# Performance work log

Measured on AMD Instinct MI355X. Metric: run time of the kernel, lower is better.

## Reference

```python
import jax, jax.numpy as jnp
import numpy as np

H = 16          # num_heads
R = 4           # query compression ratio
WIN = 128       # sliding window size
NEG = -1e9      # finite mask value (safe softmax grads)


def setup_inputs() -> dict:
    key = jax.random.key(0)
    k0, k1, k2, k3, k4 = jax.random.split(key, 5)
    B, S, D = 4, 4096, 2048
    inputs = jax.random.normal(k0, (B, S, D), jnp.float32)
    attention_mask = jnp.ones((B, S), jnp.int32)
    s = 0.02
    Wq = jax.random.normal(k1, (D, D), jnp.float32) * s
    Wk = jax.random.normal(k2, (D, D), jnp.float32) * s
    Wv = jax.random.normal(k3, (D, D), jnp.float32) * s
    Wo = jax.random.normal(k4, (D, D), jnp.float32) * s
    return {"inputs": inputs, "attention_mask": attention_mask,
            "Wq": Wq, "Wk": Wk, "Wv": Wv, "Wo": Wo}


def _forward(inputs, attention_mask, Wq, Wk, Wv, Wo):
    B, S, D = inputs.shape
    dh = D // H
    scale = 1.0 / np.sqrt(dh).astype(np.float32)
    Cs = (S + R - 1) // R            # compressed query length (S % R == 0 here)
    win = min(WIN, S)
    ws = max(0, S - win)             # window start

    # Q projection -> [B,H,S,dh] -> compress groups of R by mean -> [B,H,Cs,dh]
    q = jnp.einsum('bsd,od->bso', inputs, Wq)
    q = q.reshape(B, S, H, dh).transpose(0, 2, 1, 3)
    qc = q.reshape(B, H, Cs, R, dh).mean(axis=3)

    # K/V only over the recent window
    wx = inputs[:, ws:ws + win, :]
    k = jnp.einsum('bsd,od->bso', wx, Wk).reshape(B, win, H, dh).transpose(0, 2, 1, 3)
    v = jnp.einsum('bsd,od->bso', wx, Wv).reshape(B, win, H, dh).transpose(0, 2, 1, 3)

    scores = jnp.einsum('bhqd,bhkd->bhqk', qc, k) * scale

    # causal mask: each compressed query sits at position (i+1)*R-1
    qpos = (jnp.arange(Cs) + 1) * R - 1                     # [Cs]
    wpos = ws + jnp.arange(win)
    causal = wpos[None, :] <= qpos[:, None]
    qbw = qpos < ws                                         # queries fully before window
    causal = causal.at[:, 0].set(causal[:, 0] | qbw)
    pad_ok = (attention_mask[:, ws:ws + win] != 0)
    full = causal[None, None, :, :] & pad_ok[:, None, None, :]

    scores = jnp.where(full, scores, NEG)
    weights = jax.nn.softmax(scores, axis=-1)
    out = jnp.einsum('bhqk,bhkd->bhqd', weights, v)         # [B,H,Cs,dh]
    out = out.transpose(0, 2, 1, 3).reshape(B, Cs, D)
    out = jnp.einsum('bsd,od->bso', out, Wo)

    if Cs != S:  # linear interpolation back to seq_len (align_corners=False)
        out = jax.image.resize(out, (B, S, D), method='linear')
    return out


def reference(inputs, attention_mask, Wq, Wk, Wv, Wo):
    return _forward(inputs, attention_mask, Wq, Wk, Wv, Wo)
```

## Files before the change

### kernel.cpp

```cpp
#include <hip/hip_runtime.h>
#include <hip/hip_bf16.h>


typedef __attribute__((ext_vector_type(8))) short short8;
typedef __attribute__((ext_vector_type(4))) float f32x4;

#define QP_SLICE  (128 * 2048)
#define KV_SLICE  (512 * 2048)
#define YO_STRIDE (132 * 2048)

__device__ __forceinline__ unsigned short f2bf(float f){
  unsigned int x = __float_as_uint(f);
  return (unsigned short)((x + 0x7fffu + ((x >> 16) & 1u)) >> 16);
}
__device__ __forceinline__ float bf2f(unsigned short u){
  return __uint_as_float(((unsigned int)u) << 16);
}
__device__ __forceinline__ float bflo(unsigned int u){ return __uint_as_float(u << 16); }
__device__ __forceinline__ float bfhi(unsigned int u){ return __uint_as_float(u & 0xffff0000u); }
__device__ __forceinline__ unsigned int pk2(float lo, float hi){
  return ((unsigned int)f2bf(hi) << 16) | (unsigned int)f2bf(lo);
}
__device__ __forceinline__ short8 cvt8(float4 x, float4 y){
  union { unsigned int u[4]; short8 s; } r;
  r.u[0] = pk2(x.x, x.y); r.u[1] = pk2(x.z, x.w);
  r.u[2] = pk2(y.x, y.y); r.u[3] = pk2(y.z, y.w);
  return r.s;
}

__global__ __launch_bounds__(256) void prep_kernel(
    const float* __restrict__ inp,
    const float* __restrict__ Wq, const float* __restrict__ Wk,
    const float* __restrict__ Wv, const float* __restrict__ Wo,
    unsigned short* __restrict__ Wb,
    unsigned short* __restrict__ Awx, unsigned short* __restrict__ Aq)
{
  const int bx = blockIdx.x;
  if (bx < 8192){
    const int idx = bx * 256 + threadIdx.x;
    const int w = idx >> 19;
    const int sub = idx & 524287;
    const float* src = (w == 0) ? Wq : (w == 1) ? Wk : (w == 2) ? Wv : Wo;
    const float* p = src + (size_t)sub * 8;
    *(short8*)&Wb[(size_t)w * 4194304 + (size_t)sub * 8] =
        cvt8(*(const float4*)p, *(const float4*)(p + 4));
  } else if (bx < 8704){
    const int idx = (bx - 8192) * 256 + threadIdx.x;
    const int b = idx >> 15;
    const int j = (idx >> 8) & 127;
    const int d8 = (idx & 255) * 8;
    const float* p = inp + ((size_t)b * 4096 + 3968 + j) * 2048 + d8;
    *(short8*)&Awx[((size_t)b * 128 + j) * 2048 + d8] =
        cvt8(*(const float4*)p, *(const float4*)(p + 4));
  } else {
    const int idx = (bx - 8704) * 256 + threadIdx.x;
    const int b = idx >> 13;
    const int c = (idx >> 8) & 31;
    const int d8 = (idx & 255) * 8;
    const float* p = inp + ((size_t)b * 4096 + 3968 + 4 * c) * 2048 + d8;
    float4 x0 = *(const float4*)(p);
    float4 x1 = *(const float4*)(p + 2048);
    float4 x2 = *(const float4*)(p + 4096);
    float4 x3 = *(const float4*)(p + 6144);
    float4 y0 = *(const float4*)(p + 4);
    float4 y1 = *(const float4*)(p + 2052);
    float4 y2 = *(const float4*)(p + 4100);
    float4 y3 = *(const float4*)(p + 6148);
    float4 xm, ym;
    xm.x = 0.25f * (x0.x + x1.x + x2.x + x3.x);
    xm.y = 0.25f * (x0.y + x1.y + x2.y + x3.y);
    xm.z = 0.25f * (x0.z + x1.z + x2.z + x3.z);
    xm.w = 0.25f * (x0.w + x1.w + x2.w + x3.w);
    ym.x = 0.25f * (y0.x + y1.x + y2.x + y3.x);
    ym.y = 0.25f * (y0.y + y1.y + y2.y + y3.y);
    ym.z = 0.25f * (y0.z + y1.z + y2.z + y3.z);
    ym.w = 0.25f * (y0.w + y1.w + y2.w + y3.w);
    *(short8*)&Aq[((size_t)b * 32 + c) * 2048 + d8] = cvt8(xm, ym);
  }
}

__device__ __forceinline__ void stage_tile(
    const unsigned short* __restrict__ A, const unsigned short* __restrict__ W,
    int row0, int n0, int kt,
    unsigned short* As, unsigned short* Bs, int wid, int lane)
{
  const int r  = lane >> 3;
  const int ug = ((lane & 7) ^ r) * 8;
  #pragma unroll
  for (int i = 0; i < 4; ++i){
    const int c = wid * 4 + i;
    __builtin_amdgcn_global_load_lds(
        (const __attribute__((address_space(1))) void*)(A + (size_t)(row0 + c * 8 + r) * 2048 + kt + ug),
        (__attribute__((address_space(3))) void*)(As + c * 512),
        16, 0, 0);
    __builtin_amdgcn_global_load_lds(
        (const __attribute__((address_space(1))) void*)(W + (size_t)(n0 + c * 8 + r) * 2048 + kt + ug),
        (__attribute__((address_space(3))) void*)(Bs + c * 512),
        16, 0, 0);
  }
}

template<bool OUT_BF16>
__device__ __forceinline__ void gemm_body(
    const unsigned short* __restrict__ A, const unsigned short* __restrict__ W,
    unsigned short* __restrict__ Cb, float* __restrict__ Cf,
    int M, int row0, int n0, int kbase, int nsteps,
    unsigned short* L)
{
  const int tid  = threadIdx.x;
  const int lane = tid & 63;
  const int wid  = tid >> 6;
  const int wr = wid >> 1, wc = wid & 1;

  f32x4 acc[4][4] = {};

  stage_tile(A, W, row0, n0, kbase, L, L + 8192, wid, lane);
  int cur = 0;

  for (int t = 0; t < nsteps; ++t){
    __syncthreads();
    const int nxt = cur ^ 1;
    if (t + 1 < nsteps)
      stage_tile(A, W, row0, n0, kbase + (t + 1) * 64,
                 L + nxt * 16384, L + nxt * 16384 + 8192, wid, lane);
    const unsigned short* As = L + cur * 16384;
    const unsigned short* Bs = As + 8192;
    #pragma unroll
    for (int ks = 0; ks < 2; ++ks){
      short8 av[4], bv[4];
      const int unit = ks * 4 + (lane >> 4);
      #pragma unroll
      for (int f = 0; f < 4; ++f){
        const int row = wr * 64 + f * 16 + (lane & 15);
        av[f] = *(const short8*)&As[row * 64 + ((unit ^ (row & 7)) * 8)];
      }
      #pragma unroll
      for (int n = 0; n < 4; ++n){
        const int row = wc * 64 + n * 16 + (lane & 15);
        bv[n] = *(const short8*)&Bs[row * 64 + ((unit ^ (row & 7)) * 8)];
      }
      #pragma unroll
      for (int f = 0; f < 4; ++f)
        #pragma unroll
        for (int n = 0; n < 4; ++n)
          acc[f][n] = __builtin_amdgcn_mfma_f32_16x16x32_bf16(av[f], bv[n], acc[f][n], 0, 0, 0);
    }
    cur = nxt;
  }

  #pragma unroll
  for (int f = 0; f < 4; ++f){
    #pragma unroll
    for (int n = 0; n < 4; ++n){
      const int col = n0 + wc * 64 + n * 16 + (lane & 15);
      #pragma unroll
      for (int r = 0; r < 4; ++r){
        const int row = row0 + wr * 64 + f * 16 + (lane >> 4) * 4 + r;
        if (row < M){
          if (OUT_BF16) Cb[(size_t)row * 2048 + col] = f2bf(acc[f][n][r]);
          else          Cf[(size_t)row * 2048 + col] = acc[f][n][r];
        }
      }
    }
  }
}

__global__ __launch_bounds__(256, 2) void qkv_kernel(
    const unsigned short* __restrict__ Aq, const unsigned short* __restrict__ Awx,
    const unsigned short* __restrict__ Wb,
    unsigned short* __restrict__ Qp, unsigned short* __restrict__ Kp,
    unsigned short* __restrict__ Vp)
{
  __shared__ __align__(16) unsigned short L[32768];
  const int flat = blockIdx.x + (blockIdx.y << 4);
  const int fid  = (flat & 7) * 36 + (flat >> 3);
  const int nt = fid & 15, gy = fid >> 4;
  if (gy < 2){
    gemm_body<true>(Aq, Wb, Qp + gy * QP_SLICE, nullptr,
                    128, 0, nt * 128, gy * 1024, 16, L);
  } else if (gy < 10){
    const int idx = gy - 2, mt = idx >> 1, ksp = idx & 1;
    gemm_body<true>(Awx, Wb + 4194304, Kp + ksp * KV_SLICE, nullptr,
                    512, mt * 128, nt * 128, ksp * 1024, 16, L);
  } else {
    const int idx = gy - 10, mt = idx >> 1, ksp = idx & 1;
    gemm_body<true>(Awx, Wb + 8388608, Vp + ksp * KV_SLICE, nullptr,
                    512, mt * 128, nt * 128, ksp * 1024, 16, L);
  }
}

__global__ __launch_bounds__(256, 2) void o_kernel(
    const unsigned short* __restrict__ Ao, const unsigned short* __restrict__ Wb,
    float* __restrict__ Yop)
{
  __shared__ __align__(16) unsigned short L[32768];
  gemm_body<false>(Ao, Wb + 12582912, nullptr, Yop + (size_t)blockIdx.z * YO_STRIDE,
                   132, blockIdx.y * 128, blockIdx.x * 128, blockIdx.z * 1024, 16, L);
}

__global__ __launch_bounds__(256) void attn_kernel(
    const unsigned short* __restrict__ Qp, const unsigned short* __restrict__ Kp,
    const unsigned short* __restrict__ Vp, const int* __restrict__ amask,
    unsigned short* __restrict__ Ao)
{
  const int b = blockIdx.x >> 4;
  const int h = blockIdx.x & 15;
  __shared__ float Qs[32][129];
  __shared__ unsigned int Ks[128][65];
  __shared__ unsigned int Vs[128][65];
  __shared__ float Wt[32][132];
  __shared__ float msk[128];
  const int tid = threadIdx.x;

  for (int i = tid; i < 32 * 128; i += 256){
    int cq = i >> 7, d = i & 127;
    size_t off = (size_t)(b * 32 + cq) * 2048 + h * 128 + d;
    Qs[cq][d] = bf2f(Qp[off]) + bf2f(Qp[off + QP_SLICE]);
  }
  for (int i = tid; i < 128 * 64; i += 256){
    int j = i >> 6, du = i & 63;
    size_t off = (size_t)(b * 128 + j) * 2048 + h * 128 + du * 2;
    unsigned int k0 = *(const unsigned int*)(Kp + off);
    unsigned int k1 = *(const unsigned int*)(Kp + off + KV_SLICE);
    unsigned int v0 = *(const unsigned int*)(Vp + off);
    unsigned int v1 = *(const unsigned int*)(Vp + off + KV_SLICE);
    Ks[j][du] = pk2(bflo(k0) + bflo(k1), bfhi(k0) + bfhi(k1));
    Vs[j][du] = pk2(bflo(v0) + bflo(v1), bfhi(v0) + bfhi(v1));
  }
  if (tid < 128){
    msk[tid] = (amask[b * 4096 + 3968 + tid] != 0) ? 1.f : 0.f;
    size_t off = (size_t)(b * 128) * 2048 + h * 128 + tid;
    Ao[(size_t)(b * 33) * 2048 + h * 128 + tid] =
        f2bf(bf2f(Vp[off]) + bf2f(Vp[off + KV_SLICE]));
  }
  __syncthreads();

  const int cq = tid >> 3, jg = tid & 7;
  const int jmax = 4 * cq + 3;
  const float scale = 0.088388347648318447f;

  float s[16];
  {
    float sacc[16];
    #pragma unroll
    for (int jj = 0; jj < 16; ++jj) sacc[jj] = 0.f;
    for (int du = 0; du < 64; ++du){
      float q0 = Qs[cq][2 * du], q1 = Qs[cq][2 * du + 1];
      #pragma unroll
      for (int jj = 0; jj < 16; ++jj){
        unsigned int u = Ks[jg * 16 + jj][du];
        sacc[jj] += q0 * bflo(u) + q1 * bfhi(u);
      }
    }
    #pragma unroll
    for (int jj = 0; jj < 16; ++jj){
      int j = jg * 16 + jj;
      bool ok = (j <= jmax) && (msk[j] > 0.5f);
      s[jj] = ok ? sacc[jj] * scale : -1e9f;
    }
  }
  float m = s[0];
  #pragma unroll
  for (int jj = 1; jj < 16; ++jj) m = fmaxf(m, s[jj]);
  #pragma unroll
  for (int off = 1; off < 8; off <<= 1) m = fmaxf(m, __shfl_xor(m, off, 8));
  float sum = 0.f;
  #pragma unroll
  for (int jj = 0; jj < 16; ++jj){ s[jj] = expf(s[jj] - m); sum += s[jj]; }
  #pragma unroll
  for (int off = 1; off < 8; off <<= 1) sum += __shfl_xor(sum, off, 8);
  const float inv = 1.f / sum;
  #pragma unroll
  for (int jj = 0; jj < 16; ++jj) Wt[cq][jg * 16 + jj] = s[jj] * inv;
  __syncthreads();

  const int dg = tid & 7;
  float o[16];
  #pragma unroll
  for (int e = 0; e < 16; ++e) o[e] = 0.f;
  for (int j = 0; j < 128; ++j){
    float w = Wt[cq][j];
    #pragma unroll
    for (int du = 0; du < 8; ++du){
      unsigned int u = Vs[j][dg * 8 + du];
      o[2 * du]     += w * bflo(u);
      o[2 * du + 1] += w * bfhi(u);
    }
  }
  unsigned short* dst = Ao + (size_t)(b * 33 + 1 + cq) * 2048 + h * 128 + dg * 16;
  #pragma unroll
  for (int e = 0; e < 16; ++e) dst[e] = f2bf(o[e]);
}

__global__ __launch_bounds__(256) void resize_kernel(
    const float* __restrict__ Yop, float* __restrict__ out)
{
  const int rowid = blockIdx.x;
  const int b = rowid >> 12;
  const int i = rowid & 4095;
  float c  = i * 0.25f - 0.375f;
  float fl = floorf(c);
  int   j0 = (int)fl;
  float f  = c - fl;
  int   j1 = j0 + 1;
  j0 = max(0, min(j0, 1023));
  j1 = max(0, min(j1, 1023));
  const int ri0 = b * 33 + (j0 <= 991 ? 0 : j0 - 991);
  const int ri1 = b * 33 + (j1 <= 991 ? 0 : j1 - 991);
  const float* r0 = Yop + (size_t)ri0 * 2048;
  const float* r1 = Yop + (size_t)ri1 * 2048;
  float* op = out + (size_t)rowid * 2048;
  const int t = threadIdx.x;
  const bool same = (ri0 == ri1);
  #pragma unroll
  for (int q = 0; q < 2; ++q){
    int d = q * 1024 + t * 4;
    float4 a0 = *(const float4*)(r0 + d);
    float4 a1 = *(const float4*)(r0 + d + YO_STRIDE);
    float4 a;
    a.x = a0.x + a1.x; a.y = a0.y + a1.y; a.z = a0.z + a1.z; a.w = a0.w + a1.w;
    float4 o = a;
    if (!same){
      float4 b0 = *(const float4*)(r1 + d);
      float4 b1 = *(const float4*)(r1 + d + YO_STRIDE);
      float4 bb;
      bb.x = b0.x + b1.x; bb.y = b0.y + b1.y; bb.z = b0.z + b1.z; bb.w = b0.w + b1.w;
      o.x = a.x + f * (bb.x - a.x);
      o.y = a.y + f * (bb.y - a.y);
      o.z = a.z + f * (bb.z - a.z);
      o.w = a.w + f * (bb.w - a.w);
    }
    *(float4*)(op + d) = o;
  }
}

extern "C" void kernel_launch(void* const* d_in, const int* in_sizes, int n_in,
                              void* d_out, int out_size, void* d_ws, size_t ws_size,
                              hipStream_t stream)
{
  const float* inp   = (const float*)d_in[0];
  const int*   amask = (const int*)d_in[1];
  const float* Wq = (const float*)d_in[2];
  const float* Wk = (const float*)d_in[3];
  const float* Wv = (const float*)d_in[4];
  const float* Wo = (const float*)d_in[5];
  float* out = (float*)d_out;

  char* ws = (char*)d_ws;
  unsigned short* Wb  = (unsigned short*)(ws);
  unsigned short* Aq  = (unsigned short*)(ws + 33554432);
  unsigned short* Awx = (unsigned short*)(ws + 34078720);
  unsigned short* Qp  = (unsigned short*)(ws + 36175872);
  unsigned short* Kp  = (unsigned short*)(ws + 37224448);
  unsigned short* Vp  = (unsigned short*)(ws + 41418752);
  unsigned short* Ao  = (unsigned short*)(ws + 45613056);
  float*          Yop = (float*)(ws + 46661632);

  prep_kernel<<<8832, 256, 0, stream>>>(inp, Wq, Wk, Wv, Wo, Wb, Awx, Aq);
  qkv_kernel<<<dim3(16, 18), 256, 0, stream>>>(Aq, Awx, Wb, Qp, Kp, Vp);
  attn_kernel<<<64, 256, 0, stream>>>(Qp, Kp, Vp, amask, Ao);
  o_kernel<<<dim3(16, 2, 2), 256, 0, stream>>>(Ao, Wb, Yop);
  resize_kernel<<<16384, 256, 0, stream>>>(Yop, out);
}
```

Baseline: 112.0 us.

## Load GEMM A operand from global directly, split-K by four, raise occupancy

The GEMM body no longer stages the A tile in LDS. Each lane reads its A fragments straight from global memory, and only the weight tile is double-buffered in LDS, which halves shared memory per block. The QKV GEMM moves from split-K 2 to split-K 4, which doubles the grid to 576 blocks with an XCD-aware mapping, and launch bounds rise to 3 blocks per CU. The attention kernel now sums four partial slices instead of two. In exchange this adds more partial-sum traffic, and the uncached global A reads are repeated by each wave-column.

Measured after the change: 150.2 us. 1.34x slower.

```diff
diff --git a/kernel.cpp b/kernel.cpp
--- a/kernel.cpp
+++ b/kernel.cpp
@@ -79,20 +79,15 @@
   }
 }
 
-__device__ __forceinline__ void stage_tile(
-    const unsigned short* __restrict__ A, const unsigned short* __restrict__ W,
-    int row0, int n0, int kt,
-    unsigned short* As, unsigned short* Bs, int wid, int lane)
+__device__ __forceinline__ void stage_b(
+    const unsigned short* __restrict__ W, int n0, int kt,
+    unsigned short* Bs, int wid, int lane)
 {
   const int r  = lane >> 3;
   const int ug = ((lane & 7) ^ r) * 8;
   #pragma unroll
   for (int i = 0; i < 4; ++i){
     const int c = wid * 4 + i;
-    __builtin_amdgcn_global_load_lds(
-        (const __attribute__((address_space(1))) void*)(A + (size_t)(row0 + c * 8 + r) * 2048 + kt + ug),
-        (__attribute__((address_space(3))) void*)(As + c * 512),
-        16, 0, 0);
     __builtin_amdgcn_global_load_lds(
         (const __attribute__((address_space(1))) void*)(W + (size_t)(n0 + c * 8 + r) * 2048 + kt + ug),
         (__attribute__((address_space(3))) void*)(Bs + c * 512),
@@ -112,28 +107,32 @@
   const int wid  = tid >> 6;
   const int wr = wid >> 1, wc = wid & 1;
 
+  const unsigned short* Ar[4];
+  #pragma unroll
+  for (int f = 0; f < 4; ++f){
+    int ar = row0 + wr * 64 + f * 16 + (lane & 15);
+    if (ar > M - 1) ar = M - 1;
+    Ar[f] = A + (size_t)ar * 2048 + (lane >> 4) * 8;
+  }
+
   f32x4 acc[4][4] = {};
 
-  stage_tile(A, W, row0, n0, kbase, L, L + 8192, wid, lane);
+  stage_b(W, n0, kbase, L, wid, lane);
   int cur = 0;
 
   for (int t = 0; t < nsteps; ++t){
     __syncthreads();
-    const int nxt = cur ^ 1;
     if (t + 1 < nsteps)
-      stage_tile(A, W, row0, n0, kbase + (t + 1) * 64,
-                 L + nxt * 16384, L + nxt * 16384 + 8192, wid, lane);
-    const unsigned short* As = L + cur * 16384;
-    const unsigned short* Bs = As + 8192;
+      stage_b(W, n0, kbase + (t + 1) * 64, L + (cur ^ 1) * 8192, wid, lane);
+    const unsigned short* Bs = L + cur * 8192;
+    const int kt = kbase + t * 64;
     #pragma unroll
     for (int ks = 0; ks < 2; ++ks){
       short8 av[4], bv[4];
       const int unit = ks * 4 + (lane >> 4);
       #pragma unroll
-      for (int f = 0; f < 4; ++f){
-        const int row = wr * 64 + f * 16 + (lane & 15);
-        av[f] = *(const short8*)&As[row * 64 + ((unit ^ (row & 7)) * 8)];
-      }
+      for (int f = 0; f < 4; ++f)
+        av[f] = *(const short8*)(Ar[f] + kt + ks * 32);
       #pragma unroll
       for (int n = 0; n < 4; ++n){
         const int row = wc * 64 + n * 16 + (lane & 15);
@@ -145,7 +144,7 @@
         for (int n = 0; n < 4; ++n)
           acc[f][n] = __builtin_amdgcn_mfma_f32_16x16x32_bf16(av[f], bv[n], acc[f][n], 0, 0, 0);
     }
-    cur = nxt;
+    cur ^= 1;
   }
 
   #pragma unroll
@@ -165,35 +164,37 @@
   }
 }
 
-__global__ __launch_bounds__(256, 2) void qkv_kernel(
+__global__ __launch_bounds__(256, 3) void qkv_kernel(
     const unsigned short* __restrict__ Aq, const unsigned short* __restrict__ Awx,
     const unsigned short* __restrict__ Wb,
     unsigned short* __restrict__ Qp, unsigned short* __restrict__ Kp,
     unsigned short* __restrict__ Vp)
 {
-  __shared__ __align__(16) unsigned short L[32768];
-  const int flat = blockIdx.x + (blockIdx.y << 4);
-  const int fid  = (flat & 7) * 36 + (flat >> 3);
-  const int nt = fid & 15, gy = fid >> 4;
-  if (gy < 2){
-    gemm_body<true>(Aq, Wb, Qp + gy * QP_SLICE, nullptr,
-                    128, 0, nt * 128, gy * 1024, 16, L);
-  } else if (gy < 10){
-    const int idx = gy - 2, mt = idx >> 1, ksp = idx & 1;
+  __shared__ __align__(16) unsigned short L[16384];
+  const int flat = blockIdx.x;
+  const int xcd = flat & 7;
+  const int w   = flat >> 3;
+  const int nt  = (xcd << 1) | (w >= 36 ? 1 : 0);
+  const int g   = (w >= 36) ? w - 36 : w;
+  if (g < 4){
+    gemm_body<true>(Aq, Wb, Qp + g * QP_SLICE, nullptr,
+                    128, 0, nt * 128, g * 512, 8, L);
+  } else if (g < 20){
+    const int idx = g - 4, mt = idx >> 2, ksp = idx & 3;
     gemm_body<true>(Awx, Wb + 4194304, Kp + ksp * KV_SLICE, nullptr,
-                    512, mt * 128, nt * 128, ksp * 1024, 16, L);
+                    512, mt * 128, nt * 128, ksp * 512, 8, L);
   } else {
-    const int idx = gy - 10, mt = idx >> 1, ksp = idx & 1;
+    const int idx = g - 20, mt = idx >> 2, ksp = idx & 3;
     gemm_body<true>(Awx, Wb + 8388608, Vp + ksp * KV_SLICE, nullptr,
-                    512, mt * 128, nt * 128, ksp * 1024, 16, L);
-  }
-}
-
-__global__ __launch_bounds__(256, 2) void o_kernel(
+                    512, mt * 128, nt * 128, ksp * 512, 8, L);
+  }
+}
+
+__global__ __launch_bounds__(256, 3) void o_kernel(
     const unsigned short* __restrict__ Ao, const unsigned short* __restrict__ Wb,
     float* __restrict__ Yop)
 {
-  __shared__ __align__(16) unsigned short L[32768];
+  __shared__ __align__(16) unsigned short L[16384];
   gemm_body<false>(Ao, Wb + 12582912, nullptr, Yop + (size_t)blockIdx.z * YO_STRIDE,
                    132, blockIdx.y * 128, blockIdx.x * 128, blockIdx.z * 1024, 16, L);
 }
@@ -215,23 +216,31 @@
   for (int i = tid; i < 32 * 128; i += 256){
     int cq = i >> 7, d = i & 127;
     size_t off = (size_t)(b * 32 + cq) * 2048 + h * 128 + d;
-    Qs[cq][d] = bf2f(Qp[off]) + bf2f(Qp[off + QP_SLICE]);
+    Qs[cq][d] = bf2f(Qp[off]) + bf2f(Qp[off + QP_SLICE]) +
+                bf2f(Qp[off + 2 * QP_SLICE]) + bf2f(Qp[off + 3 * QP_SLICE]);
   }
   for (int i = tid; i < 128 * 64; i += 256){
     int j = i >> 6, du = i & 63;
     size_t off = (size_t)(b * 128 + j) * 2048 + h * 128 + du * 2;
     unsigned int k0 = *(const unsigned int*)(Kp + off);
     unsigned int k1 = *(const unsigned int*)(Kp + off + KV_SLICE);
+    unsigned int k2 = *(const unsigned int*)(Kp + off + 2 * KV_SLICE);
+    unsigned int k3 = *(const unsigned int*)(Kp + off + 3 * KV_SLICE);
     unsigned int v0 = *(const unsigned int*)(Vp + off);
     unsigned int v1 = *(const unsigned int*)(Vp + off + KV_SLICE);
-    Ks[j][du] = pk2(bflo(k0) + bflo(k1), bfhi(k0) + bfhi(k1));
-    Vs[j][du] = pk2(bflo(v0) + bflo(v1), bfhi(v0) + bfhi(v1));
+    unsigned int v2 = *(const unsigned int*)(Vp + off + 2 * KV_SLICE);
+    unsigned int v3 = *(const unsigned int*)(Vp + off + 3 * KV_SLICE);
+    Ks[j][du] = pk2(bflo(k0) + bflo(k1) + bflo(k2) + bflo(k3),
+                    bfhi(k0) + bfhi(k1) + bfhi(k2) + bfhi(k3));
+    Vs[j][du] = pk2(bflo(v0) + bflo(v1) + bflo(v2) + bflo(v3),
+                    bfhi(v0) + bfhi(v1) + bfhi(v2) + bfhi(v3));
   }
   if (tid < 128){
     msk[tid] = (amask[b * 4096 + 3968 + tid] != 0) ? 1.f : 0.f;
     size_t off = (size_t)(b * 128) * 2048 + h * 128 + tid;
     Ao[(size_t)(b * 33) * 2048 + h * 128 + tid] =
-        f2bf(bf2f(Vp[off]) + bf2f(Vp[off + KV_SLICE]));
+        f2bf(bf2f(Vp[off]) + bf2f(Vp[off + KV_SLICE]) +
+             bf2f(Vp[off + 2 * KV_SLICE]) + bf2f(Vp[off + 3 * KV_SLICE]));
   }
   __syncthreads();
 
@@ -351,13 +360,13 @@
   unsigned short* Aq  = (unsigned short*)(ws + 33554432);
   unsigned short* Awx = (unsigned short*)(ws + 34078720);
   unsigned short* Qp  = (unsigned short*)(ws + 36175872);
-  unsigned short* Kp  = (unsigned short*)(ws + 37224448);
-  unsigned short* Vp  = (unsigned short*)(ws + 41418752);
-  unsigned short* Ao  = (unsigned short*)(ws + 45613056);
-  float*          Yop = (float*)(ws + 46661632);
+  unsigned short* Kp  = (unsigned short*)(ws + 38273024);
+  unsigned short* Vp  = (unsigned short*)(ws + 46661632);
+  unsigned short* Ao  = (unsigned short*)(ws + 55050240);
+  float*          Yop = (float*)(ws + 56098816);
 
   prep_kernel<<<8832, 256, 0, stream>>>(inp, Wq, Wk, Wv, Wo, Wb, Awx, Aq);
-  qkv_kernel<<<dim3(16, 18), 256, 0, stream>>>(Aq, Awx, Wb, Qp, Kp, Vp);
+  qkv_kernel<<<576, 256, 0, stream>>>(Aq, Awx, Wb, Qp, Kp, Vp);
   attn_kernel<<<64, 256, 0, stream>>>(Qp, Kp, Vp, amask, Ao);
   o_kernel<<<dim3(16, 2, 2), 256, 0, stream>>>(Ao, Wb, Yop);
   resize_kernel<<<16384, 256, 0, stream>>>(Yop, out);
```

## Switch GEMM staging to four-deep K=32 ring buffer with vmcnt waits

Applied to the files above, without the earlier changes.

The GEMM main loop now stages K-slices of 32 instead of 64 into a 4-slot LDS ring, keeping two tiles in flight ahead of compute. Partial s_waitcnt vmcnt counts plus a raw s_barrier replace the full __syncthreads, so global loads for later tiles can overlap MFMA work on the current one. Step counts double to cover the same K range. In exchange there is one barrier per 32-wide K step instead of per 64, and the raw barrier and hand-picked vmcnt values depend on correct wait accounting to avoid read hazards.

New measurement: 116.1 us. 1.04x slower.

```diff
diff --git a/kernel.cpp b/kernel.cpp
--- a/kernel.cpp
+++ b/kernel.cpp
@@ -79,23 +79,23 @@
   }
 }
 
-__device__ __forceinline__ void stage_tile(
+__device__ __forceinline__ void stage32(
     const unsigned short* __restrict__ A, const unsigned short* __restrict__ W,
     int row0, int n0, int kt,
-    unsigned short* As, unsigned short* Bs, int wid, int lane)
-{
-  const int r  = lane >> 3;
-  const int ug = ((lane & 7) ^ r) * 8;
-  #pragma unroll
-  for (int i = 0; i < 4; ++i){
-    const int c = wid * 4 + i;
+    unsigned short* buf, int wid, int lane)
+{
+  #pragma unroll
+  for (int i = 0; i < 2; ++i){
+    const int rbase = (wid << 5) + i * 16;
+    const int r = rbase + (lane >> 2);
+    const int ug = ((lane & 3) ^ (r & 3)) * 8;
     __builtin_amdgcn_global_load_lds(
-        (const __attribute__((address_space(1))) void*)(A + (size_t)(row0 + c * 8 + r) * 2048 + kt + ug),
-        (__attribute__((address_space(3))) void*)(As + c * 512),
+        (const __attribute__((address_space(1))) void*)(A + (size_t)(row0 + r) * 2048 + kt + ug),
+        (__attribute__((address_space(3))) void*)(buf + rbase * 32),
         16, 0, 0);
     __builtin_amdgcn_global_load_lds(
-        (const __attribute__((address_space(1))) void*)(W + (size_t)(n0 + c * 8 + r) * 2048 + kt + ug),
-        (__attribute__((address_space(3))) void*)(Bs + c * 512),
+        (const __attribute__((address_space(1))) void*)(W + (size_t)(n0 + r) * 2048 + kt + ug),
+        (__attribute__((address_space(3))) void*)(buf + 4096 + rbase * 32),
         16, 0, 0);
   }
 }
@@ -114,38 +114,37 @@
 
   f32x4 acc[4][4] = {};
 
-  stage_tile(A, W, row0, n0, kbase, L, L + 8192, wid, lane);
-  int cur = 0;
+  stage32(A, W, row0, n0, kbase,      L,        wid, lane);
+  stage32(A, W, row0, n0, kbase + 32, L + 8192, wid, lane);
 
   for (int t = 0; t < nsteps; ++t){
-    __syncthreads();
-    const int nxt = cur ^ 1;
-    if (t + 1 < nsteps)
-      stage_tile(A, W, row0, n0, kbase + (t + 1) * 64,
-                 L + nxt * 16384, L + nxt * 16384 + 8192, wid, lane);
-    const unsigned short* As = L + cur * 16384;
-    const unsigned short* Bs = As + 8192;
-    #pragma unroll
-    for (int ks = 0; ks < 2; ++ks){
-      short8 av[4], bv[4];
-      const int unit = ks * 4 + (lane >> 4);
+    if (t + 2 < nsteps)
+      stage32(A, W, row0, n0, kbase + (t + 2) * 32, L + ((t + 2) & 3) * 8192, wid, lane);
+    if (t + 2 < nsteps)      asm volatile("s_waitcnt vmcnt(8)" ::: "memory");
+    else if (t + 1 < nsteps) asm volatile("s_waitcnt vmcnt(4)" ::: "memory");
+    else                     asm volatile("s_waitcnt vmcnt(0)" ::: "memory");
+    __builtin_amdgcn_s_barrier();
+    __builtin_amdgcn_sched_barrier(0);
+
+    const unsigned short* As = L + (t & 3) * 8192;
+    const unsigned short* Bs = As + 4096;
+    const int u = lane >> 4;
+    short8 av[4], bv[4];
+    #pragma unroll
+    for (int f = 0; f < 4; ++f){
+      const int row = wr * 64 + f * 16 + (lane & 15);
+      av[f] = *(const short8*)&As[row * 32 + ((u ^ (row & 3)) * 8)];
+    }
+    #pragma unroll
+    for (int n = 0; n < 4; ++n){
+      const int row = wc * 64 + n * 16 + (lane & 15);
+      bv[n] = *(const short8*)&Bs[row * 32 + ((u ^ (row & 3)) * 8)];
+    }
+    #pragma unroll
+    for (int f = 0; f < 4; ++f)
       #pragma unroll
-      for (int f = 0; f < 4; ++f){
-        const int row = wr * 64 + f * 16 + (lane & 15);
-        av[f] = *(const short8*)&As[row * 64 + ((unit ^ (row & 7)) * 8)];
-      }
-      #pragma unroll
-      for (int n = 0; n < 4; ++n){
-        const int row = wc * 64 + n * 16 + (lane & 15);
-        bv[n] = *(const short8*)&Bs[row * 64 + ((unit ^ (row & 7)) * 8)];
-      }
-      #pragma unroll
-      for (int f = 0; f < 4; ++f)
-        #pragma unroll
-        for (int n = 0; n < 4; ++n)
-          acc[f][n] = __builtin_amdgcn_mfma_f32_16x16x32_bf16(av[f], bv[n], acc[f][n], 0, 0, 0);
-    }
-    cur = nxt;
+      for (int n = 0; n < 4; ++n)
+        acc[f][n] = __builtin_amdgcn_mfma_f32_16x16x32_bf16(av[f], bv[n], acc[f][n], 0, 0, 0);
   }
 
   #pragma unroll
@@ -177,15 +176,15 @@
   const int nt = fid & 15, gy = fid >> 4;
   if (gy < 2){
     gemm_body<true>(Aq, Wb, Qp + gy * QP_SLICE, nullptr,
-                    128, 0, nt * 128, gy * 1024, 16, L);
+                    128, 0, nt * 128, gy * 1024, 32, L);
   } else if (gy < 10){
     const int idx = gy - 2, mt = idx >> 1, ksp = idx & 1;
     gemm_body<true>(Awx, Wb + 4194304, Kp + ksp * KV_SLICE, nullptr,
-                    512, mt * 128, nt * 128, ksp * 1024, 16, L);
+                    512, mt * 128, nt * 128, ksp * 1024, 32, L);
   } else {
     const int idx = gy - 10, mt = idx >> 1, ksp = idx & 1;
     gemm_body<true>(Awx, Wb + 8388608, Vp + ksp * KV_SLICE, nullptr,
-                    512, mt * 128, nt * 128, ksp * 1024, 16, L);
+                    512, mt * 128, nt * 128, ksp * 1024, 32, L);
   }
 }
 
@@ -195,7 +194,7 @@
 {
   __shared__ __align__(16) unsigned short L[32768];
   gemm_body<false>(Ao, Wb + 12582912, nullptr, Yop + (size_t)blockIdx.z * YO_STRIDE,
-                   132, blockIdx.y * 128, blockIdx.x * 128, blockIdx.z * 1024, 16, L);
+                   132, blockIdx.y * 128, blockIdx.x * 128, blockIdx.z * 1024, 32, L);
 }
 
 __global__ __launch_bounds__(256) void attn_kernel(
```
